# Optimization experiments

Hardware: AMD Instinct MI355X
Metric: run time of the kernel (lower is better)

The kernel has to match this reference:

```python
import jax, jax.numpy as jnp
import numpy as np

N = 100000       # nodes
DEG = 16         # fixed out/in degree used to build CSR
E = N * DEG      # edges
D_IN = 128       # in_feats
D_OUT = 256      # out_feats
K = 32           # maxk k_value


def _xavier_uniform(key, shape, gain):
    fan_out, fan_in = shape
    bound = gain * np.sqrt(6.0 / (fan_in + fan_out))
    return jax.random.uniform(key, shape, jnp.float32, -bound, bound)


def setup_inputs() -> dict:
    key = jax.random.key(0)
    ks = jax.random.split(key, 6)
    feat = jax.random.normal(ks[0], (N, D_IN), jnp.float32)
    topk_values = jax.random.uniform(ks[1], (N, K), jnp.float32)
    topk_indices = jax.random.randint(ks[2], (N, K), 0, D_IN).astype(jnp.int32)
    # CSR graph: fixed degree -> indptr is arange*DEG; random destinations
    indptr = (jnp.arange(N + 1) * DEG).astype(jnp.int32)
    indices = jax.random.randint(ks[3], (E,), 0, N).astype(jnp.int32)
    # set_graph_data: csr weight[e] = 1 / clamp(in_degree(dst), 1)
    in_deg = jax.ops.segment_sum(jnp.ones(E, jnp.float32), indices, num_segments=N)
    in_deg = jnp.maximum(in_deg, 1.0)
    csr_values = 1.0 / in_deg[indices]
    gain = np.sqrt(2.0)  # calculate_gain('relu')
    w_neigh = _xavier_uniform(ks[4], (D_OUT, D_IN), gain)
    w_self = _xavier_uniform(ks[5], (D_OUT, D_IN), gain)
    b_self = jnp.zeros((D_OUT,), jnp.float32)
    return {"feat": feat, "topk_values": topk_values, "csr_values": csr_values,
            "w_neigh": w_neigh, "w_self": w_self, "b_self": b_self,
            "topk_indices": topk_indices, "indptr": indptr, "indices": indices}


def reference(feat, topk_values, csr_values, w_neigh, w_self, b_self,
              topk_indices, indptr, indices):
    # Densify the k-sparse MaxK features: x[n, topk_indices[n, j]] = topk_values[n, j]
    x = jnp.zeros((N, D_IN), feat.dtype).at[
        jnp.arange(N)[:, None], topk_indices].add(topk_values)
    # Edge-weight-normalized SpMM over CSR: out[row] += w[e] * x[col[e]]
    row_ids = jnp.repeat(jnp.arange(N), jnp.diff(indptr), total_repeat_length=E)
    msgs = x[indices] * csr_values[:, None]          # [E, D_IN]
    agg = jax.ops.segment_sum(msgs, row_ids, num_segments=N)  # [N, D_IN]
    # lin_before_mp is False (in_feats <= out_feats): project after aggregation
    h_neigh = agg @ w_neigh.T                        # [N, D_OUT]
    rst = feat @ w_self.T + b_self + h_neigh         # fc_self(h_self) + h_neigh
    return rst
```

## Files before the change

### kernel.cpp

```cpp
#include <hip/hip_runtime.h>
#include <hip/hip_bf16.h>
#include <stdint.h>

#define N_NODES 100000
#define DEG 16
#define D_IN 128
#define D_OUT 256
#define K_TOP 32
#define K_CAT 256

typedef __attribute__((ext_vector_type(8))) short short8;
typedef __attribute__((ext_vector_type(4))) float floatx4;

__device__ __forceinline__ unsigned pack_bf16_rne(float f) {
    union { float f; unsigned u; } c; c.f = f;
    unsigned u = c.u;
    return (u + 0x7fffu + ((u >> 16) & 1u)) >> 16;
}
__device__ __forceinline__ float bf16lo_to_f(unsigned lo16) {
    union { unsigned u; float f; } c; c.u = lo16 << 16; return c.f;
}

typedef __attribute__((address_space(1))) void as1_void;
typedef __attribute__((address_space(3))) void as3_void;
__device__ __forceinline__ void gload_lds16(const void* g, void* l) {
    __builtin_amdgcn_global_load_lds((as1_void*)g, (as3_void*)l, 16, 0, 0);
}

__global__ __launch_bounds__(256) void k_packw(const float* __restrict__ w_self,
                                               const float* __restrict__ w_neigh,
                                               unsigned short* __restrict__ bmat) {
    int o = blockIdx.x;
    int k = threadIdx.x;
    float v = (k < D_IN) ? w_self[o * D_IN + k] : w_neigh[o * D_IN + (k - D_IN)];
    bmat[o * K_CAT + k] = (unsigned short)pack_bf16_rne(v);
}

#define DROWS 64
__global__ __launch_bounds__(256) void k_densify(const float* __restrict__ topk_v,
                                                 const int* __restrict__ topk_i,
                                                 const float* __restrict__ feat,
                                                 unsigned short* __restrict__ xbf,
                                                 unsigned short* __restrict__ fbf) {
    __shared__ float sx[DROWS * D_IN];
    const int t = threadIdx.x;
    const int row0 = blockIdx.x * DROWS;

    #pragma unroll
    for (int p = 0; p < 8; ++p)
        *(floatx4*)&sx[(t + p * 256) * 4] = (floatx4){0.f, 0.f, 0.f, 0.f};
    __syncthreads();

    const size_t tbase = (size_t)row0 * K_TOP;
    #pragma unroll
    for (int p = 0; p < 8; ++p) {
        int q = t + p * 256;
        int r = q >> 5;
        if (row0 + r < N_NODES) {
            int   ci = topk_i[tbase + q];
            float cv = topk_v[tbase + q];
            atomicAdd(&sx[r * D_IN + ci], cv);
        }
    }
    __syncthreads();

    #pragma unroll
    for (int p = 0; p < 16; ++p) {
        int d = t + p * 256;
        int r = d >> 6;
        int c2 = (d & 63) * 2;
        if (row0 + r < N_NODES) {
            float2 v = *(const float2*)&sx[r * D_IN + c2];
            ((unsigned*)(xbf + (size_t)(row0 + r) * D_IN))[d & 63] =
                pack_bf16_rne(v.x) | (pack_bf16_rne(v.y) << 16);
        }
    }

    #pragma unroll
    for (int p = 0; p < 8; ++p) {
        int q = t + p * 256;
        int r = q >> 5;
        int c4 = (q & 31) * 4;
        if (row0 + r < N_NODES) {
            float4 f = *(const float4*)(feat + (size_t)(row0 + r) * D_IN + c4);
            uint2 pk;
            pk.x = pack_bf16_rne(f.x) | (pack_bf16_rne(f.y) << 16);
            pk.y = pack_bf16_rne(f.z) | (pack_bf16_rne(f.w) << 16);
            ((uint2*)(fbf + (size_t)(row0 + r) * D_IN))[q & 31] = pk;
        }
    }
}

#define BM 128
#define BN 256
#define BK 32
#define NTA 4
#define NT  8

__global__ __launch_bounds__(512, 2) void k_fused(const float* __restrict__ csr_w,
                                                  const int* __restrict__ col_idx,
                                                  const unsigned short* __restrict__ xbf,
                                                  const unsigned short* __restrict__ fbf,
                                                  const unsigned short* __restrict__ bmat,
                                                  const float* __restrict__ bias,
                                                  float* __restrict__ out) {
    __shared__ __align__(16) unsigned short Agg[BM * 128];
    __shared__ __align__(16) unsigned short As[2][BM * BK];
    __shared__ __align__(16) unsigned short Bs[2][BN * BK];
    const int t    = threadIdx.x;
    const int lane = t & 63, wave = t >> 6;
    const int l16  = lane & 15, quad = lane >> 4;
    const int row0 = blockIdx.x * BM;

    const int a_r = wave * 16 + (lane >> 2);
    const int a_c = (lane & 3) * 8;
    int a_gr = row0 + a_r; if (a_gr >= N_NODES) a_gr = N_NODES - 1;
    const unsigned short* gA  = fbf  + (size_t)a_gr * D_IN + a_c;
    const unsigned short* gB0 = bmat + (size_t)a_r        * K_CAT + a_c;
    const unsigned short* gB1 = bmat + (size_t)(a_r + 128) * K_CAT + a_c;

#define STAGE_A(buf, tt) gload_lds16(gA + (tt) * BK, &As[buf][wave * 16 * BK])
#define STAGE_B(buf, tt) do {                                                 \
        gload_lds16(gB0 + (tt) * BK, &Bs[buf][(wave * 16)       * BK]);       \
        gload_lds16(gB1 + (tt) * BK, &Bs[buf][(wave * 16 + 128) * BK]);       \
    } while (0)

    STAGE_A(0, 0);
    STAGE_B(0, 0);

    const int ql = lane & 15, qb = lane & 48;
    #pragma unroll 1
    for (int p = 0; p < 4; ++p) {
        const int r  = p * 32 + wave * 4 + (lane >> 4);
        const int gr = row0 + r;
        int   c = 0; float w = 0.f;
        if (gr < N_NODES) {
            c = col_idx[gr * DEG + ql];
            w = csr_w [gr * DEG + ql];
        }
        uint4 vv[DEG];
        #pragma unroll
        for (int e = 0; e < DEG; ++e) {
            int col = __shfl(c, qb | e);
            vv[e] = *(const uint4*)(xbf + (size_t)col * D_IN + ql * 8);
        }
        float a[8] = {0.f, 0.f, 0.f, 0.f, 0.f, 0.f, 0.f, 0.f};
        #pragma unroll
        for (int e = 0; e < DEG; ++e) {
            float we = __shfl(w, qb | e);
            uint4 v = vv[e];
            a[0] += we * bf16lo_to_f(v.x & 0xffffu);
            a[1] += we * bf16lo_to_f(v.x >> 16);
            a[2] += we * bf16lo_to_f(v.y & 0xffffu);
            a[3] += we * bf16lo_to_f(v.y >> 16);
            a[4] += we * bf16lo_to_f(v.z & 0xffffu);
            a[5] += we * bf16lo_to_f(v.z >> 16);
            a[6] += we * bf16lo_to_f(v.w & 0xffffu);
            a[7] += we * bf16lo_to_f(v.w >> 16);
        }
        uint4 pk;
        pk.x = pack_bf16_rne(a[0]) | (pack_bf16_rne(a[1]) << 16);
        pk.y = pack_bf16_rne(a[2]) | (pack_bf16_rne(a[3]) << 16);
        pk.z = pack_bf16_rne(a[4]) | (pack_bf16_rne(a[5]) << 16);
        pk.w = pack_bf16_rne(a[6]) | (pack_bf16_rne(a[7]) << 16);
        *(uint4*)&Agg[r * 128 + ((ql * 8) ^ ((r & 7) << 3))] = pk;
    }

    const int wr = wave >> 2, wc = wave & 3;
    floatx4 acc[4][4];
    #pragma unroll
    for (int i = 0; i < 4; ++i)
        #pragma unroll
        for (int j = 0; j < 4; ++j)
            acc[i][j] = (floatx4){0.f, 0.f, 0.f, 0.f};

    __syncthreads();

    #pragma unroll
    for (int tt = 0; tt < NT; ++tt) {
        const int cur = tt & 1;
        if (tt + 1 < NTA) STAGE_A(cur ^ 1, tt + 1);
        if (tt + 1 < NT)  STAGE_B(cur ^ 1, tt + 1);

        short8 afr[4], bfr[4];
        if (tt < NTA) {
            #pragma unroll
            for (int i = 0; i < 4; ++i)
                afr[i] = *(const short8*)&As[cur][(wr * 64 + i * 16 + l16) * BK + quad * 8];
        } else {
            const int c0 = (tt - NTA) * 32 + quad * 8;
            #pragma unroll
            for (int i = 0; i < 4; ++i) {
                const int m = wr * 64 + i * 16 + l16;
                afr[i] = *(const short8*)&Agg[m * 128 + (c0 ^ ((m & 7) << 3))];
            }
        }
        #pragma unroll
        for (int j = 0; j < 4; ++j)
            bfr[j] = *(const short8*)&Bs[cur][(wc * 64 + j * 16 + l16) * BK + quad * 8];

        #pragma unroll
        for (int i = 0; i < 4; ++i)
            #pragma unroll
            for (int j = 0; j < 4; ++j)
                acc[i][j] = __builtin_amdgcn_mfma_f32_16x16x32_bf16(bfr[j], afr[i], acc[i][j], 0, 0, 0);

        if (tt + 1 < NT) __syncthreads();
    }

    #pragma unroll
    for (int j = 0; j < 4; ++j) {
        const int cg = wc * 64 + j * 16 + quad * 4;
        const float4 bv = *(const float4*)&bias[cg];
        #pragma unroll
        for (int i = 0; i < 4; ++i) {
            const int gr = row0 + wr * 64 + i * 16 + l16;
            if (gr < N_NODES) {
                float4 v;
                v.x = acc[i][j][0] + bv.x;
                v.y = acc[i][j][1] + bv.y;
                v.z = acc[i][j][2] + bv.z;
                v.w = acc[i][j][3] + bv.w;
                *(float4*)(out + (size_t)gr * D_OUT + cg) = v;
            }
        }
    }
#undef STAGE_A
#undef STAGE_B
}

extern "C" void kernel_launch(void* const* d_in, const int* in_sizes, int n_in,
                              void* d_out, int out_size, void* d_ws, size_t ws_size,
                              hipStream_t stream) {
    const float* feat    = (const float*)d_in[0];
    const float* topk_v  = (const float*)d_in[1];
    const float* csr_w   = (const float*)d_in[2];
    const float* w_neigh = (const float*)d_in[3];
    const float* w_self  = (const float*)d_in[4];
    const float* b_self  = (const float*)d_in[5];
    const int*   topk_i  = (const int*)d_in[6];
    const int*   indices = (const int*)d_in[8];
    float* out = (float*)d_out;

    unsigned short* xbf  = (unsigned short*)d_ws;
    unsigned short* fbf  = xbf + (size_t)N_NODES * D_IN;
    unsigned short* bmat = fbf + (size_t)N_NODES * D_IN;

    k_packw<<<dim3(256), dim3(256), 0, stream>>>(w_self, w_neigh, bmat);
    k_densify<<<dim3((N_NODES + DROWS - 1) / DROWS), dim3(256), 0, stream>>>(topk_v, topk_i, feat, xbf, fbf);
    k_fused<<<dim3((N_NODES + BM - 1) / BM), dim3(512), 0, stream>>>(csr_w, indices, xbf, fbf, bmat, b_self, out);
}
```

Measured before the change: 296.2 us.

## Gather sparse top-k records instead of dense rows and merge prep kernels

Stops densifying the MaxK features. A prep kernel now packs each node's 32 top-k values (bf16) and indices (u8) into a 96-byte record. The fused kernel gathers these compact records per edge and scatters them into an fp32 LDS aggregation buffer with shared-memory atomics, in two 64-row passes. The goal is to cut gather bytes from 256 to 96 per neighbor and to drop the dense xbf write and read. The cost is many LDS atomics, with possible contention, plus extra syncs. Packing of the weights, feat and records is merged into one launch, LDS is reused between the aggregation and GEMM staging buffers, and the occupancy hint is raised to 4.

After: 544.1 us. 1.84x slower.

```diff
diff --git a/kernel.cpp b/kernel.cpp
--- a/kernel.cpp
+++ b/kernel.cpp
@@ -27,67 +27,61 @@
     __builtin_amdgcn_global_load_lds((as1_void*)g, (as3_void*)l, 16, 0, 0);
 }
 
-__global__ __launch_bounds__(256) void k_packw(const float* __restrict__ w_self,
-                                               const float* __restrict__ w_neigh,
-                                               unsigned short* __restrict__ bmat) {
-    int o = blockIdx.x;
-    int k = threadIdx.x;
-    float v = (k < D_IN) ? w_self[o * D_IN + k] : w_neigh[o * D_IN + (k - D_IN)];
-    bmat[o * K_CAT + k] = (unsigned short)pack_bf16_rne(v);
-}
-
-#define DROWS 64
-__global__ __launch_bounds__(256) void k_densify(const float* __restrict__ topk_v,
-                                                 const int* __restrict__ topk_i,
-                                                 const float* __restrict__ feat,
-                                                 unsigned short* __restrict__ xbf,
-                                                 unsigned short* __restrict__ fbf) {
-    __shared__ float sx[DROWS * D_IN];
+#define FEAT_BLKS 1563
+#define PACK_BLKS 1563
+
+__global__ __launch_bounds__(256) void k_prep(const float* __restrict__ feat,
+                                              const float* __restrict__ topk_v,
+                                              const int* __restrict__ topk_i,
+                                              const float* __restrict__ w_self,
+                                              const float* __restrict__ w_neigh,
+                                              unsigned short* __restrict__ fbf,
+                                              unsigned char* __restrict__ pkrec,
+                                              unsigned short* __restrict__ bmat) {
     const int t = threadIdx.x;
-    const int row0 = blockIdx.x * DROWS;
-
-    #pragma unroll
-    for (int p = 0; p < 8; ++p)
-        *(floatx4*)&sx[(t + p * 256) * 4] = (floatx4){0.f, 0.f, 0.f, 0.f};
-    __syncthreads();
-
-    const size_t tbase = (size_t)row0 * K_TOP;
-    #pragma unroll
-    for (int p = 0; p < 8; ++p) {
-        int q = t + p * 256;
-        int r = q >> 5;
-        if (row0 + r < N_NODES) {
-            int   ci = topk_i[tbase + q];
-            float cv = topk_v[tbase + q];
-            atomicAdd(&sx[r * D_IN + ci], cv);
-        }
-    }
-    __syncthreads();
-
-    #pragma unroll
-    for (int p = 0; p < 16; ++p) {
-        int d = t + p * 256;
-        int r = d >> 6;
-        int c2 = (d & 63) * 2;
-        if (row0 + r < N_NODES) {
-            float2 v = *(const float2*)&sx[r * D_IN + c2];
-            ((unsigned*)(xbf + (size_t)(row0 + r) * D_IN))[d & 63] =
-                pack_bf16_rne(v.x) | (pack_bf16_rne(v.y) << 16);
-        }
-    }
-
-    #pragma unroll
-    for (int p = 0; p < 8; ++p) {
-        int q = t + p * 256;
-        int r = q >> 5;
-        int c4 = (q & 31) * 4;
-        if (row0 + r < N_NODES) {
-            float4 f = *(const float4*)(feat + (size_t)(row0 + r) * D_IN + c4);
-            uint2 pk;
-            pk.x = pack_bf16_rne(f.x) | (pack_bf16_rne(f.y) << 16);
-            pk.y = pack_bf16_rne(f.z) | (pack_bf16_rne(f.w) << 16);
-            ((uint2*)(fbf + (size_t)(row0 + r) * D_IN))[q & 31] = pk;
-        }
+    const int bid = blockIdx.x;
+    if (bid < FEAT_BLKS) {
+        const int row0 = bid * 64;
+        #pragma unroll
+        for (int p = 0; p < 8; ++p) {
+            int q = t + p * 256;
+            int r = q >> 5;
+            int c4 = (q & 31) * 4;
+            if (row0 + r < N_NODES) {
+                float4 f = *(const float4*)(feat + (size_t)(row0 + r) * D_IN + c4);
+                uint2 pv;
+                pv.x = pack_bf16_rne(f.x) | (pack_bf16_rne(f.y) << 16);
+                pv.y = pack_bf16_rne(f.z) | (pack_bf16_rne(f.w) << 16);
+                ((uint2*)(fbf + (size_t)(row0 + r) * D_IN))[q & 31] = pv;
+            }
+        }
+    } else if (bid < FEAT_BLKS + PACK_BLKS) {
+        const int n = (bid - FEAT_BLKS) * 64 + (t >> 2);
+        const int p = t & 3;
+        if (n < N_NODES) {
+            const float* vs = topk_v + (size_t)n * K_TOP + p * 8;
+            float4 v0 = ((const float4*)vs)[0];
+            float4 v1 = ((const float4*)vs)[1];
+            const int* is = topk_i + (size_t)n * K_TOP + p * 8;
+            int4 i0 = ((const int4*)is)[0];
+            int4 i1 = ((const int4*)is)[1];
+            uint4 pv;
+            pv.x = pack_bf16_rne(v0.x) | (pack_bf16_rne(v0.y) << 16);
+            pv.y = pack_bf16_rne(v0.z) | (pack_bf16_rne(v0.w) << 16);
+            pv.z = pack_bf16_rne(v1.x) | (pack_bf16_rne(v1.y) << 16);
+            pv.w = pack_bf16_rne(v1.z) | (pack_bf16_rne(v1.w) << 16);
+            uint2 pi;
+            pi.x = (unsigned)i0.x | ((unsigned)i0.y << 8) | ((unsigned)i0.z << 16) | ((unsigned)i0.w << 24);
+            pi.y = (unsigned)i1.x | ((unsigned)i1.y << 8) | ((unsigned)i1.z << 16) | ((unsigned)i1.w << 24);
+            unsigned char* rec = pkrec + (size_t)n * 96;
+            *(uint4*)(rec + p * 16) = pv;
+            *(uint2*)(rec + 64 + p * 8) = pi;
+        }
+    } else {
+        const int o = bid - (FEAT_BLKS + PACK_BLKS);
+        const int k = t;
+        float v = (k < D_IN) ? w_self[o * D_IN + k] : w_neigh[o * D_IN + (k - D_IN)];
+        bmat[o * K_CAT + k] = (unsigned short)pack_bf16_rne(v);
     }
 }
 
@@ -97,19 +91,22 @@
 #define NTA 4
 #define NT  8
 
-__global__ __launch_bounds__(512, 2) void k_fused(const float* __restrict__ csr_w,
+__global__ __launch_bounds__(512, 4) void k_fused(const float* __restrict__ csr_w,
                                                   const int* __restrict__ col_idx,
-                                                  const unsigned short* __restrict__ xbf,
+                                                  const unsigned char* __restrict__ pkrec,
                                                   const unsigned short* __restrict__ fbf,
                                                   const unsigned short* __restrict__ bmat,
                                                   const float* __restrict__ bias,
                                                   float* __restrict__ out) {
-    __shared__ __align__(16) unsigned short Agg[BM * 128];
-    __shared__ __align__(16) unsigned short As[2][BM * BK];
-    __shared__ __align__(16) unsigned short Bs[2][BN * BK];
-    const int t    = threadIdx.x;
+    __shared__ __align__(16) char smem[81920];
+    unsigned short* aggbf = (unsigned short*)smem;
+    float* aggf = (float*)(smem + 32768);
+    unsigned short (*As)[BM * BK] = (unsigned short (*)[BM * BK])(smem + 32768);
+    unsigned short (*Bs)[BN * BK] = (unsigned short (*)[BN * BK])(smem + 49152);
+
+    const int t = threadIdx.x;
     const int lane = t & 63, wave = t >> 6;
-    const int l16  = lane & 15, quad = lane >> 4;
+    const int l16 = lane & 15, quad = lane >> 4;
     const int row0 = blockIdx.x * BM;
 
     const int a_r = wave * 16 + (lane >> 2);
@@ -125,48 +122,57 @@
         gload_lds16(gB1 + (tt) * BK, &Bs[buf][(wave * 16 + 128) * BK]);       \
     } while (0)
 
+    STAGE_B(1, 0);
+
+    #pragma unroll
+    for (int p = 0; p < 4; ++p)
+        *(floatx4*)&aggf[(t + p * 512) * 4] = (floatx4){0.f, 0.f, 0.f, 0.f};
+    __syncthreads();
+
+    #pragma unroll 1
+    for (int pass = 0; pass < 2; ++pass) {
+        const int rbase = row0 + pass * 64;
+        const int ebase = rbase * DEG;
+        #pragma unroll 4
+        for (int s = 0; s < 8; ++s) {
+            int q = s * 512 + t;
+            int e = q >> 2;
+            int p = q & 3;
+            int lr = e >> 4;
+            if (rbase + lr < N_NODES) {
+                int   col = col_idx[ebase + e];
+                float w   = csr_w [ebase + e];
+                const unsigned char* rec = pkrec + (size_t)col * 96;
+                uint4 v  = *(const uint4*)(rec + p * 16);
+                uint2 id = *(const uint2*)(rec + 64 + p * 8);
+                float* arow = aggf + lr * D_IN;
+                atomicAdd(&arow[ id.x        & 255], w * bf16lo_to_f(v.x & 0xffffu));
+                atomicAdd(&arow[(id.x >>  8) & 255], w * bf16lo_to_f(v.x >> 16));
+                atomicAdd(&arow[(id.x >> 16) & 255], w * bf16lo_to_f(v.y & 0xffffu));
+                atomicAdd(&arow[ id.x >> 24       ], w * bf16lo_to_f(v.y >> 16));
+                atomicAdd(&arow[ id.y        & 255], w * bf16lo_to_f(v.z & 0xffffu));
+                atomicAdd(&arow[(id.y >>  8) & 255], w * bf16lo_to_f(v.z >> 16));
+                atomicAdd(&arow[(id.y >> 16) & 255], w * bf16lo_to_f(v.w & 0xffffu));
+                atomicAdd(&arow[ id.y >> 24       ], w * bf16lo_to_f(v.w >> 16));
+            }
+        }
+        __syncthreads();
+        #pragma unroll
+        for (int s = 0; s < 8; ++s) {
+            int d  = s * 512 + t;
+            int lr = d >> 6;
+            int c2 = (d & 63) * 2;
+            float2 v = *(const float2*)&aggf[lr * D_IN + c2];
+            int R = pass * 64 + lr;
+            *(unsigned*)&aggbf[R * D_IN + (c2 ^ ((R & 7) << 3))] =
+                pack_bf16_rne(v.x) | (pack_bf16_rne(v.y) << 16);
+            if (pass == 0) *(float2*)&aggf[lr * D_IN + c2] = make_float2(0.f, 0.f);
+        }
+        __syncthreads();
+    }
+
     STAGE_A(0, 0);
-    STAGE_B(0, 0);
-
-    const int ql = lane & 15, qb = lane & 48;
-    #pragma unroll 1
-    for (int p = 0; p < 4; ++p) {
-        const int r  = p * 32 + wave * 4 + (lane >> 4);
-        const int gr = row0 + r;
-        int   c = 0; float w = 0.f;
-        if (gr < N_NODES) {
-            c = col_idx[gr * DEG + ql];
-            w = csr_w [gr * DEG + ql];
-        }
-        uint4 vv[DEG];
-        #pragma unroll
-        for (int e = 0; e < DEG; ++e) {
-            int col = __shfl(c, qb | e);
-            vv[e] = *(const uint4*)(xbf + (size_t)col * D_IN + ql * 8);
-        }
-        float a[8] = {0.f, 0.f, 0.f, 0.f, 0.f, 0.f, 0.f, 0.f};
-        #pragma unroll
-        for (int e = 0; e < DEG; ++e) {
-            float we = __shfl(w, qb | e);
-            uint4 v = vv[e];
-            a[0] += we * bf16lo_to_f(v.x & 0xffffu);
-            a[1] += we * bf16lo_to_f(v.x >> 16);
-            a[2] += we * bf16lo_to_f(v.y & 0xffffu);
-            a[3] += we * bf16lo_to_f(v.y >> 16);
-            a[4] += we * bf16lo_to_f(v.z & 0xffffu);
-            a[5] += we * bf16lo_to_f(v.z >> 16);
-            a[6] += we * bf16lo_to_f(v.w & 0xffffu);
-            a[7] += we * bf16lo_to_f(v.w >> 16);
-        }
-        uint4 pk;
-        pk.x = pack_bf16_rne(a[0]) | (pack_bf16_rne(a[1]) << 16);
-        pk.y = pack_bf16_rne(a[2]) | (pack_bf16_rne(a[3]) << 16);
-        pk.z = pack_bf16_rne(a[4]) | (pack_bf16_rne(a[5]) << 16);
-        pk.w = pack_bf16_rne(a[6]) | (pack_bf16_rne(a[7]) << 16);
-        *(uint4*)&Agg[r * 128 + ((ql * 8) ^ ((r & 7) << 3))] = pk;
-    }
-
-    const int wr = wave >> 2, wc = wave & 3;
+
     floatx4 acc[4][4];
     #pragma unroll
     for (int i = 0; i < 4; ++i)
@@ -176,11 +182,12 @@
 
     __syncthreads();
 
+    const int wr = wave >> 2, wc = wave & 3;
     #pragma unroll
     for (int tt = 0; tt < NT; ++tt) {
         const int cur = tt & 1;
         if (tt + 1 < NTA) STAGE_A(cur ^ 1, tt + 1);
-        if (tt + 1 < NT)  STAGE_B(cur ^ 1, tt + 1);
+        if (tt + 1 < NT)  STAGE_B(cur, tt + 1);
 
         short8 afr[4], bfr[4];
         if (tt < NTA) {
@@ -192,12 +199,12 @@
             #pragma unroll
             for (int i = 0; i < 4; ++i) {
                 const int m = wr * 64 + i * 16 + l16;
-                afr[i] = *(const short8*)&Agg[m * 128 + (c0 ^ ((m & 7) << 3))];
+                afr[i] = *(const short8*)&aggbf[m * 128 + (c0 ^ ((m & 7) << 3))];
             }
         }
         #pragma unroll
         for (int j = 0; j < 4; ++j)
-            bfr[j] = *(const short8*)&Bs[cur][(wc * 64 + j * 16 + l16) * BK + quad * 8];
+            bfr[j] = *(const short8*)&Bs[cur ^ 1][(wc * 64 + j * 16 + l16) * BK + quad * 8];
 
         #pragma unroll
         for (int i = 0; i < 4; ++i)
@@ -242,11 +249,13 @@
     const int*   indices = (const int*)d_in[8];
     float* out = (float*)d_out;
 
-    unsigned short* xbf  = (unsigned short*)d_ws;
-    unsigned short* fbf  = xbf + (size_t)N_NODES * D_IN;
-    unsigned short* bmat = fbf + (size_t)N_NODES * D_IN;
-
-    k_packw<<<dim3(256), dim3(256), 0, stream>>>(w_self, w_neigh, bmat);
-    k_densify<<<dim3((N_NODES + DROWS - 1) / DROWS), dim3(256), 0, stream>>>(topk_v, topk_i, feat, xbf, fbf);
-    k_fused<<<dim3((N_NODES + BM - 1) / BM), dim3(512), 0, stream>>>(csr_w, indices, xbf, fbf, bmat, b_self, out);
-}
+    unsigned char* base = (unsigned char*)d_ws;
+    unsigned short* fbf   = (unsigned short*)base;
+    unsigned char*  pkrec = base + (size_t)N_NODES * D_IN * 2;
+    unsigned short* bmat  = (unsigned short*)(pkrec + (size_t)N_NODES * 96);
+
+    k_prep<<<dim3(FEAT_BLKS + PACK_BLKS + 256), dim3(256), 0, stream>>>(
+        feat, topk_v, topk_i, w_self, w_neigh, fbf, pkrec, bmat);
+    k_fused<<<dim3((N_NODES + BM - 1) / BM), dim3(512), 0, stream>>>(
+        csr_w, indices, pkrec, fbf, bmat, b_self, out);
+}
```
